# Kernel tuning notes

Measured on AMD Instinct MI355X. Metric: run time of the kernel, lower is better.

The kernel has to match this reference:

```python
import jax, jax.numpy as jnp
import numpy as np

LN_EPS = 1e-3  # keras LayerNormalization default


def setup_inputs() -> dict:
    key = jax.random.key(0)
    k1, k2, k3 = jax.random.split(key, 3)
    B, T, D, H = 64, 512, 256, 512
    inputs = jax.random.normal(k1, (B, T, D), dtype=jnp.float32)
    h0 = jnp.zeros((B, H), dtype=jnp.float32)
    Wx = jax.random.normal(k2, (D, H), dtype=jnp.float32) / np.sqrt(D)
    Wh = jax.random.normal(k3, (H, H), dtype=jnp.float32) / np.sqrt(H)
    b = jnp.zeros((H,), dtype=jnp.float32)
    gamma = jnp.ones((H,), dtype=jnp.float32)
    beta = jnp.zeros((H,), dtype=jnp.float32)
    return {"inputs": inputs, "h0": h0, "Wx": Wx, "Wh": Wh, "b": b,
            "gamma": gamma, "beta": beta}


def _layer_norm(x, gamma, beta):
    mu = jnp.mean(x, axis=-1, keepdims=True)
    var = jnp.mean(jnp.square(x - mu), axis=-1, keepdims=True)
    return (x - mu) * jax.lax.rsqrt(var + LN_EPS) * gamma + beta


def reference(inputs, h0, Wx, Wh, b, gamma, beta):
    # Precompute input projection for all timesteps: [B, T, H]
    xproj = jnp.einsum('btd,dh->bth', inputs, Wx) + b

    def step(h, xp_t):
        z = xp_t + h @ Wh                      # SimpleRNNCell, activation=None
        h_new = jnp.tanh(_layer_norm(z, gamma, beta))
        return h_new, h_new

    _, outs = jax.lax.scan(step, h0, jnp.swapaxes(xproj, 0, 1))
    return jnp.swapaxes(outs, 0, 1)            # [B, T, H]
```

## Files before the change

kernel.cpp:

```cpp
#include <hip/hip_runtime.h>
#include <cstdint>
#include <cstddef>

#define T_STEPS 512
#define D_DIM 256
#define H_DIM 512
#define B_SZ 64

#define NCG 4
#define CGW (H_DIM / NCG)
#define NTH 512


#define BM 64
#define BN 128
#define BK 32

__global__ __launch_bounds__(256)
void xproj_gemm(const float* __restrict__ A, const float* __restrict__ Bm,
                const float* __restrict__ bias, float* __restrict__ C,
                int M, int N, int K) {
    __shared__ float As[BK][BM];
    __shared__ float Bs[BK][BN];

    const int tid = threadIdx.x;
    const int tx = tid & 15;
    const int ty = tid >> 4;
    const int row0 = blockIdx.y * BM;
    const int col0 = blockIdx.x * BN;

    float acc[4][8];
    #pragma unroll
    for (int i = 0; i < 4; ++i)
        #pragma unroll
        for (int j = 0; j < 8; ++j) acc[i][j] = 0.0f;

    for (int kt = 0; kt < K; kt += BK) {
        #pragma unroll
        for (int i = 0; i < 2; ++i) {
            int q  = tid + i * 256;
            int m  = q >> 3;
            int k4 = (q & 7) << 2;
            float4 v = *(const float4*)&A[(size_t)(row0 + m) * K + kt + k4];
            As[k4 + 0][m] = v.x; As[k4 + 1][m] = v.y;
            As[k4 + 2][m] = v.z; As[k4 + 3][m] = v.w;
        }
        #pragma unroll
        for (int i = 0; i < 4; ++i) {
            int q  = tid + i * 256;
            int kk = q >> 5;
            int n4 = (q & 31) << 2;
            *(float4*)&Bs[kk][n4] = *(const float4*)&Bm[(size_t)(kt + kk) * N + col0 + n4];
        }
        __syncthreads();
        #pragma unroll
        for (int k = 0; k < BK; ++k) {
            float4 a  = *(const float4*)&As[k][ty << 2];
            float4 b0 = *(const float4*)&Bs[k][tx << 2];
            float4 b1 = *(const float4*)&Bs[k][(tx << 2) + 64];
            float av[4] = {a.x, a.y, a.z, a.w};
            float bv[8] = {b0.x, b0.y, b0.z, b0.w, b1.x, b1.y, b1.z, b1.w};
            #pragma unroll
            for (int i = 0; i < 4; ++i)
                #pragma unroll
                for (int j = 0; j < 8; ++j)
                    acc[i][j] = fmaf(av[i], bv[j], acc[i][j]);
        }
        __syncthreads();
    }

    float bv0[4], bv1[4];
    #pragma unroll
    for (int j = 0; j < 4; ++j) {
        bv0[j] = bias[col0 + (tx << 2) + j];
        bv1[j] = bias[col0 + (tx << 2) + 64 + j];
    }
    #pragma unroll
    for (int i = 0; i < 4; ++i) {
        int r = row0 + (ty << 2) + i;
        float4 o0 = make_float4(acc[i][0] + bv0[0], acc[i][1] + bv0[1],
                                acc[i][2] + bv0[2], acc[i][3] + bv0[3]);
        float4 o1 = make_float4(acc[i][4] + bv1[0], acc[i][5] + bv1[1],
                                acc[i][6] + bv1[2], acc[i][7] + bv1[3]);
        *(float4*)&C[(size_t)r * N + col0 + (tx << 2)]      = o0;
        *(float4*)&C[(size_t)r * N + col0 + (tx << 2) + 64] = o1;
    }
}

__device__ __forceinline__ float tanh_fast(float x) {
    float ax = fabsf(x);
    float e  = __expf(2.0f * ax);
    float t  = 1.0f - 2.0f / (e + 1.0f);
    return copysignf(t, x);
}

__global__ __launch_bounds__(NTH)
void rnn_scan3(const float* __restrict__ Wh, const float* __restrict__ h0,
               const float* __restrict__ gamma, const float* __restrict__ beta,
               float* __restrict__ out,
               unsigned long long* __restrict__ zbuf) {
    const int r   = blockIdx.x & (B_SZ - 1);
    const int cg  = blockIdx.x >> 6;
    const int tid = threadIdx.x;
    const int c   = tid & (CGW - 1);
    const int kc  = tid >> 7;

    __shared__ float h_s[H_DIM];
    __shared__ float part_s[NCG][CGW];
    __shared__ float wred_s[16];

    float w[128];
    #pragma unroll
    for (int j = 0; j < 128; ++j)
        w[j] = Wh[(size_t)(kc * 128 + j) * H_DIM + cg * CGW + c];

    h_s[tid] = h0[r * H_DIM + tid];
    const float g_own = gamma[tid];
    const float b_own = beta[tid];
    float* outrow = out + (size_t)r * T_STEPS * H_DIM;
    unsigned long long* zrow0 = zbuf + (size_t)(r * 2) * H_DIM;
    __syncthreads();

    for (int t = 0; t < T_STEPS; ++t) {
        unsigned long long* zrow = zrow0 + (size_t)(t & 1) * H_DIM;
        const unsigned int tag = (unsigned int)(t + 1);

        float xp = 0.0f;
        if (tid < CGW) xp = outrow[t * H_DIM + cg * CGW + tid];

        float acc = 0.0f;
        const float4* h4 = (const float4*)&h_s[kc * 128];
        #pragma unroll
        for (int j4 = 0; j4 < 32; ++j4) {
            float4 hv = h4[j4];
            acc = fmaf(w[4 * j4 + 0], hv.x, acc);
            acc = fmaf(w[4 * j4 + 1], hv.y, acc);
            acc = fmaf(w[4 * j4 + 2], hv.z, acc);
            acc = fmaf(w[4 * j4 + 3], hv.w, acc);
        }
        part_s[kc][c] = acc;
        __syncthreads();

        if (tid < CGW) {
            float z = xp + part_s[0][tid] + part_s[1][tid]
                         + part_s[2][tid] + part_s[3][tid];
            unsigned long long pkt =
                ((unsigned long long)tag << 32) | (unsigned long long)__float_as_uint(z);
            __hip_atomic_store(&zrow[cg * CGW + tid], pkt,
                               __ATOMIC_RELAXED, __HIP_MEMORY_SCOPE_AGENT);
        }

        unsigned long long pkt;
        do {
            pkt = __hip_atomic_load(&zrow[tid], __ATOMIC_RELAXED,
                                    __HIP_MEMORY_SCOPE_AGENT);
        } while ((unsigned int)(pkt >> 32) != tag);
        float z = __uint_as_float((unsigned int)pkt);

        float s = z, q = z * z;
        #pragma unroll
        for (int o = 32; o > 0; o >>= 1) {
            s += __shfl_down(s, o, 64);
            q += __shfl_down(q, o, 64);
        }
        const int wid = tid >> 6;
        if ((tid & 63) == 0) { wred_s[wid] = s; wred_s[8 + wid] = q; }
        __syncthreads();
        float S = 0.0f, Q = 0.0f;
        #pragma unroll
        for (int i = 0; i < 8; ++i) { S += wred_s[i]; Q += wred_s[8 + i]; }
        float mean = S * (1.0f / H_DIM);
        float var  = Q * (1.0f / H_DIM) - mean * mean;
        float rstd = rsqrtf(var + 1e-3f);

        float hn = tanh_fast((z - mean) * rstd * g_own + b_own);
        if (kc == cg) outrow[t * H_DIM + tid] = hn;
        h_s[tid] = hn;
        __syncthreads();
    }
}

extern "C" void kernel_launch(void* const* d_in, const int* in_sizes, int n_in,
                              void* d_out, int out_size, void* d_ws, size_t ws_size,
                              hipStream_t stream) {
    const float* inputs = (const float*)d_in[0];
    const float* h0     = (const float*)d_in[1];
    const float* Wx     = (const float*)d_in[2];
    const float* Wh     = (const float*)d_in[3];
    const float* bias   = (const float*)d_in[4];
    const float* gamma  = (const float*)d_in[5];
    const float* beta   = (const float*)d_in[6];
    float* out = (float*)d_out;

    unsigned long long* zbuf = (unsigned long long*)d_ws;

    const int M = B_SZ * T_STEPS;
    dim3 g1(H_DIM / BN, M / BM);
    xproj_gemm<<<g1, 256, 0, stream>>>(inputs, Wx, bias, out, M, H_DIM, D_DIM);

    rnn_scan3<<<B_SZ * NCG, NTH, 0, stream>>>(Wh, h0, gamma, beta, out, zbuf);
}
```

Baseline: 1.243 ms.

## Run RNN scan in one block per batch row with fp16 dot2 weights

Measured after the change: 1.854 ms. +49.1%, slower.

```diff
diff --git a/kernel.cpp b/kernel.cpp
--- a/kernel.cpp
+++ b/kernel.cpp
@@ -1,4 +1,5 @@
 #include <hip/hip_runtime.h>
+#include <hip/hip_fp16.h>
 #include <cstdint>
 #include <cstddef>
 
@@ -7,10 +8,9 @@
 #define H_DIM 512
 #define B_SZ 64
 
-#define NCG 4
-#define CGW (H_DIM / NCG)
-#define NTH 512
-
+#define NTH5 1024
+#define WREG 92
+#define WLDS 18
 
 #define BM 64
 #define BN 128
@@ -87,6 +87,18 @@
     }
 }
 
+typedef _Float16 half2v __attribute__((ext_vector_type(2)));
+
+__device__ __forceinline__ float fdot2u(unsigned int a, unsigned int b, float c) {
+    return __builtin_amdgcn_fdot2(__builtin_bit_cast(half2v, a),
+                                  __builtin_bit_cast(half2v, b), c, false);
+}
+
+__device__ __forceinline__ unsigned int pack_h2(float lo, float hi) {
+    __half2 h = __floats2half2_rn(lo, hi);
+    return __builtin_bit_cast(unsigned int, h);
+}
+
 __device__ __forceinline__ float tanh_fast(float x) {
     float ax = fabsf(x);
     float e  = __expf(2.0f * ax);
@@ -94,77 +106,83 @@
     return copysignf(t, x);
 }
 
-__global__ __launch_bounds__(NTH)
-void rnn_scan3(const float* __restrict__ Wh, const float* __restrict__ h0,
+__global__ __launch_bounds__(NTH5, 4)
+void rnn_scan5(const float* __restrict__ Wh, const float* __restrict__ h0,
                const float* __restrict__ gamma, const float* __restrict__ beta,
-               float* __restrict__ out,
-               unsigned long long* __restrict__ zbuf) {
-    const int r   = blockIdx.x & (B_SZ - 1);
-    const int cg  = blockIdx.x >> 6;
+               float* __restrict__ out) {
+    const int r   = blockIdx.x;
     const int tid = threadIdx.x;
-    const int c   = tid & (CGW - 1);
-    const int kc  = tid >> 7;
-
-    __shared__ float h_s[H_DIM];
-    __shared__ float part_s[NCG][CGW];
+    const int c   = tid & (H_DIM - 1);
+    const int kh  = tid >> 9;
+
+    __shared__ uint2 wl2[WLDS][NTH5];
+    __shared__ __align__(16) __half hh_s[H_DIM];
+    __shared__ float part_s[NTH5];
     __shared__ float wred_s[16];
 
-    float w[128];
-    #pragma unroll
-    for (int j = 0; j < 128; ++j)
-        w[j] = Wh[(size_t)(kc * 128 + j) * H_DIM + cg * CGW + c];
-
-    h_s[tid] = h0[r * H_DIM + tid];
-    const float g_own = gamma[tid];
-    const float b_own = beta[tid];
+    unsigned int wreg[WREG];
+    {
+        const float* wcol = Wh + (size_t)(kh * 256) * H_DIM + c;
+        #pragma unroll
+        for (int j = 0; j < WREG; ++j) {
+            float w0 = wcol[(size_t)(2 * j    ) * H_DIM];
+            float w1 = wcol[(size_t)(2 * j + 1) * H_DIM];
+            wreg[j] = pack_h2(w0, w1);
+        }
+        #pragma unroll
+        for (int p = 0; p < WLDS; ++p) {
+            int j0 = WREG + 2 * p;
+            float a0 = wcol[(size_t)(2 * j0    ) * H_DIM];
+            float a1 = wcol[(size_t)(2 * j0 + 1) * H_DIM];
+            float a2 = wcol[(size_t)(2 * j0 + 2) * H_DIM];
+            float a3 = wcol[(size_t)(2 * j0 + 3) * H_DIM];
+            wl2[p][tid] = make_uint2(pack_h2(a0, a1), pack_h2(a2, a3));
+        }
+    }
+    if (tid < H_DIM) hh_s[tid] = __float2half_rn(h0[r * H_DIM + tid]);
+    const float g_own = (tid < H_DIM) ? gamma[tid] : 0.0f;
+    const float b_own = (tid < H_DIM) ? beta[tid]  : 0.0f;
     float* outrow = out + (size_t)r * T_STEPS * H_DIM;
-    unsigned long long* zrow0 = zbuf + (size_t)(r * 2) * H_DIM;
     __syncthreads();
 
     for (int t = 0; t < T_STEPS; ++t) {
-        unsigned long long* zrow = zrow0 + (size_t)(t & 1) * H_DIM;
-        const unsigned int tag = (unsigned int)(t + 1);
-
-        float xp = 0.0f;
-        if (tid < CGW) xp = outrow[t * H_DIM + cg * CGW + tid];
-
+        float xp = (tid < H_DIM) ? outrow[t * H_DIM + tid] : 0.0f;
+
+        const uint4* hu4 = ((const uint4*)hh_s) + kh * 32;
+        const uint2* hu2 = ((const uint2*)hh_s) + kh * 64 + (WREG >> 1);
         float acc = 0.0f;
-        const float4* h4 = (const float4*)&h_s[kc * 128];
-        #pragma unroll
-        for (int j4 = 0; j4 < 32; ++j4) {
-            float4 hv = h4[j4];
-            acc = fmaf(w[4 * j4 + 0], hv.x, acc);
-            acc = fmaf(w[4 * j4 + 1], hv.y, acc);
-            acc = fmaf(w[4 * j4 + 2], hv.z, acc);
-            acc = fmaf(w[4 * j4 + 3], hv.w, acc);
-        }
-        part_s[kc][c] = acc;
-        __syncthreads();
-
-        if (tid < CGW) {
-            float z = xp + part_s[0][tid] + part_s[1][tid]
-                         + part_s[2][tid] + part_s[3][tid];
-            unsigned long long pkt =
-                ((unsigned long long)tag << 32) | (unsigned long long)__float_as_uint(z);
-            __hip_atomic_store(&zrow[cg * CGW + tid], pkt,
-                               __ATOMIC_RELAXED, __HIP_MEMORY_SCOPE_AGENT);
-        }
-
-        unsigned long long pkt;
-        do {
-            pkt = __hip_atomic_load(&zrow[tid], __ATOMIC_RELAXED,
-                                    __HIP_MEMORY_SCOPE_AGENT);
-        } while ((unsigned int)(pkt >> 32) != tag);
-        float z = __uint_as_float((unsigned int)pkt);
-
-        float s = z, q = z * z;
+        #pragma unroll
+        for (int j4 = 0; j4 < WREG / 4; ++j4) {
+            uint4 hv = hu4[j4];
+            acc = fdot2u(wreg[4 * j4 + 0], hv.x, acc);
+            acc = fdot2u(wreg[4 * j4 + 1], hv.y, acc);
+            acc = fdot2u(wreg[4 * j4 + 2], hv.z, acc);
+            acc = fdot2u(wreg[4 * j4 + 3], hv.w, acc);
+        }
+        #pragma unroll
+        for (int p = 0; p < WLDS; ++p) {
+            uint2 wv = wl2[p][tid];
+            uint2 hv = hu2[p];
+            acc = fdot2u(wv.x, hv.x, acc);
+            acc = fdot2u(wv.y, hv.y, acc);
+        }
+        part_s[tid] = acc;
+        __syncthreads();
+
+        float z = 0.0f, s = 0.0f, q = 0.0f;
+        if (tid < H_DIM) {
+            z = part_s[tid] + part_s[tid + H_DIM] + xp;
+            s = z; q = z * z;
+        }
         #pragma unroll
         for (int o = 32; o > 0; o >>= 1) {
             s += __shfl_down(s, o, 64);
             q += __shfl_down(q, o, 64);
         }
-        const int wid = tid >> 6;
-        if ((tid & 63) == 0) { wred_s[wid] = s; wred_s[8 + wid] = q; }
+        if (tid < H_DIM && (tid & 63) == 0) {
+            wred_s[tid >> 6]     = s;
+            wred_s[8 + (tid >> 6)] = q;
+        }
         __syncthreads();
         float S = 0.0f, Q = 0.0f;
         #pragma unroll
@@ -173,9 +191,11 @@
         float var  = Q * (1.0f / H_DIM) - mean * mean;
         float rstd = rsqrtf(var + 1e-3f);
 
-        float hn = tanh_fast((z - mean) * rstd * g_own + b_own);
-        if (kc == cg) outrow[t * H_DIM + tid] = hn;
-        h_s[tid] = hn;
+        if (tid < H_DIM) {
+            float hn = tanh_fast((z - mean) * rstd * g_own + b_own);
+            outrow[t * H_DIM + tid] = hn;
+            hh_s[tid] = __float2half_rn(hn);
+        }
         __syncthreads();
     }
 }
@@ -192,11 +212,9 @@
     const float* beta   = (const float*)d_in[6];
     float* out = (float*)d_out;
 
-    unsigned long long* zbuf = (unsigned long long*)d_ws;
-
     const int M = B_SZ * T_STEPS;
     dim3 g1(H_DIM / BN, M / BM);
     xproj_gemm<<<g1, 256, 0, stream>>>(inputs, Wx, bias, out, M, H_DIM, D_DIM);
 
-    rnn_scan3<<<B_SZ * NCG, NTH, 0, stream>>>(Wh, h0, gamma, beta, out, zbuf);
-}
+    rnn_scan5<<<B_SZ, NTH5, 0, stream>>>(Wh, h0, gamma, beta, out);
+}
```
